# Kernel optimization log

Measured on AMD Instinct MI355X. Metric: run time of the kernel, lower is better.

The kernel has to match this reference:

```python
import jax, jax.numpy as jnp
import numpy as np
from jax import lax

H = 64
V = 32000
B = 32
T = 512


def setup_inputs() -> dict:
    key = jax.random.key(0)
    k1, k2, k3, k4 = jax.random.split(key, 4)
    # Parameters, constructed exactly as in SOHMM.__init__
    alpha_exp = jax.nn.softmax(jax.random.normal(k1, (H, H, H), dtype=jnp.float32), axis=2)
    beta = jax.nn.log_softmax(jax.random.normal(k2, (H, V), dtype=jnp.float32), axis=1)
    gamma = jax.nn.log_softmax(jax.random.normal(k3, (H, H), dtype=jnp.float32).reshape(-1)).reshape(H, H)
    input_ids = jax.random.randint(k4, (B, T), 0, V, dtype=jnp.int64)
    return {"alpha_exp": alpha_exp, "beta": beta, "gamma": gamma, "input_ids": input_ids}


def reference(alpha_exp, beta, gamma, input_ids):
    # input_ids: [B, T]
    h = alpha_exp.shape[0]
    b, t = input_ids.shape
    ids = input_ids.T  # [T, B]
    mask = (ids != -1)
    # emission log-probs per timestep: [T, H, B]; -1 padding tokens zeroed
    ip = jnp.transpose(beta[:, jnp.where(mask, ids, 0)], (1, 0, 2)) * mask[:, None, :].astype(beta.dtype)
    gamma_exp = jax.nn.softmax(gamma.reshape(-1)).reshape(gamma.shape)

    # t = T-1: y starts at zeros then adds emission
    y0 = jnp.zeros((h, h, b), dtype=beta.dtype) + ip[-1][None, :, :]

    def step(y, ip_t):
        y_max = y.max(axis=(0, 1), keepdims=True)            # [1,1,B]
        y_exp = jnp.exp(y - y_max)
        y = jnp.log(jnp.einsum('ijk,jkb->ijb', alpha_exp, y_exp)) + y_max
        y = y + ip_t[None, :, :]
        return y, y

    # loop t = T-2 .. 0 (reverse over remaining emissions)
    y_last, ys_rest = lax.scan(step, y0, ip[:-1][::-1])
    ys = jnp.concatenate([y0[None], ys_rest], axis=0)       # [T, H, H, B]

    y_max = y_last.max(axis=(0, 1))                          # [B]
    final = jnp.log(jnp.einsum('ij,ijb->b', gamma_exp, jnp.exp(y_last - y_max[None, None, :]))) + y_max
    return ys, final
```

## Files before the change

kernel.cpp:

```cpp
#include <hip/hip_runtime.h>
#include <cstdint>
#include <cstddef>

#define Hh 64
#define Vv 32000
#define Bb 32
#define Tt 512

typedef _Float16 half2_t __attribute__((ext_vector_type(2)));

#define IP_OFF    0ull
#define IP_SZ     ((size_t)Bb*Tt*Hh*4)
#define SL_OFF    (IP_OFF + IP_SZ)
#define SL_SZ     ((size_t)Bb*Tt*4)
#define DM_OFF    (SL_OFF + SL_SZ)
#define DM_SZ     ((size_t)Bb*Tt*4)
#define U511_OFF  (DM_OFF + DM_SZ)
#define U511_SZ   ((size_t)Bb*Hh*Hh*4)
#define STAGE_OFF (U511_OFF + U511_SZ)
#define STAGE_SZ  ((size_t)Tt*Bb*Hh*Hh*2)

__device__ __forceinline__ float wave_max64(float v){
  #pragma unroll
  for (int off=32; off; off>>=1) v = fmaxf(v, __shfl_xor(v, off, 64));
  return v;
}

__device__ __forceinline__ half2_t pk16(float x, float y){
  return __builtin_bit_cast(half2_t, __builtin_amdgcn_cvt_pkrtz(x, y));
}

__global__ __launch_bounds__(256) void sohmm_ipfill(
    const float* __restrict__ beta, const int* __restrict__ ids,
    float* __restrict__ ipbuf, float* __restrict__ dmax)
{
  const int bid = blockIdx.x;
  const int b = bid >> 7, tq = bid & 127;
  const int t = tq*4 + (threadIdx.x >> 6);
  const int j = threadIdx.x & 63;
  const int id = ids[b*Tt + t];
  float ip = beta[(size_t)j*Vv + id];
  ipbuf[((size_t)b*Tt + t)*Hh + j] = ip;
  float m = wave_max64(ip);
  if (j == 0) dmax[b*Tt + t] = m;
}

__global__ __launch_bounds__(512)
void sohmm_scan(
    const float* __restrict__ alpha, const float* __restrict__ ipbuf,
    const float* __restrict__ dmax,
    float* __restrict__ out, float* __restrict__ SL,
    float* __restrict__ u511, unsigned int* __restrict__ stage, int use_stage)
{
  const int b    = blockIdx.x;
  const int tid  = threadIdx.x;
  const int j    = tid >> 3;
  const int igrp = tid & 7;
  const int w    = tid >> 6;
  const int lane = tid & 63;
  const int i0   = igrp * 8;

  __shared__ char zb[2][64*128];
  __shared__ char aL[512*272];
  __shared__ float wred[2][8];

  half2_t areg[6][32];
  #pragma unroll
  for (int m=0; m<6; m++){
    const float4* ap = (const float4*)(alpha + (((size_t)(i0+m))*Hh + j)*Hh);
    #pragma unroll
    for (int q=0; q<16; q++){
      float4 v = ap[q];
      areg[m][2*q+0] = pk16(v.x, v.y);
      areg[m][2*q+1] = pk16(v.z, v.w);
    }
  }
  #pragma unroll
  for (int mm=0; mm<2; mm++){
    const float4* ap = (const float4*)(alpha + (((size_t)(i0+6+mm))*Hh + j)*Hh);
    #pragma unroll
    for (int q=0; q<8; q++){
      float4 v0 = ap[2*q], v1 = ap[2*q+1];
      uint4 u;
      u.x = __builtin_bit_cast(unsigned, __builtin_amdgcn_cvt_pkrtz(v0.x, v0.y));
      u.y = __builtin_bit_cast(unsigned, __builtin_amdgcn_cvt_pkrtz(v0.z, v0.w));
      u.z = __builtin_bit_cast(unsigned, __builtin_amdgcn_cvt_pkrtz(v1.x, v1.y));
      u.w = __builtin_bit_cast(unsigned, __builtin_amdgcn_cvt_pkrtz(v1.z, v1.w));
      *(uint4*)(aL + (size_t)tid*272 + mm*128 + q*16) = u;
    }
  }
  __syncthreads();

  const int kzj = ((j >> 3) ^ j) & 7;
  const int jc  = j >> 3;
  const int jo  = (j & 7) * 2;

  float logC = 0.f;

  for (int s=0; s<Tt; s++){
    const int cs = s & 1, ps = cs ^ 1;
    const int t  = (Tt-1) - s;

    float ipv = ipbuf[((size_t)b*Tt + t)*Hh + j];
    float dmv = dmax[b*Tt + t];

    float y[8];

    if (s){
      uint4 w0 = *(const uint4*)(&wred[ps][0]);
      uint4 w1 = *(const uint4*)(&wred[ps][4]);
      float Mprev = fmaxf(
        fmaxf(fmaxf(__uint_as_float(w0.x),__uint_as_float(w0.y)),
              fmaxf(__uint_as_float(w0.z),__uint_as_float(w0.w))),
        fmaxf(fmaxf(__uint_as_float(w1.x),__uint_as_float(w1.y)),
              fmaxf(__uint_as_float(w1.z),__uint_as_float(w1.w))));

      float acc[8];
      #pragma unroll
      for (int m=0;m<8;m++) acc[m] = 0.f;

      const char* zrow = zb[ps] + j*128;
      const char* arow = aL + (size_t)tid*272;
      #pragma unroll
      for (int h=0; h<2; h++){
        unsigned zz[16];
        #pragma unroll
        for (int c=0; c<4; c++){
          uint4 zq = *(const uint4*)(zrow + (((h*4+c) ^ kzj) << 4));
          zz[4*c+0]=zq.x; zz[4*c+1]=zq.y; zz[4*c+2]=zq.z; zz[4*c+3]=zq.w;
        }
        #pragma unroll
        for (int m=0; m<6; m++){
          #pragma unroll
          for (int p=0; p<16; p++)
            acc[m] = __builtin_amdgcn_fdot2(areg[m][16*h+p],
                       __builtin_bit_cast(half2_t, zz[p]), acc[m], false);
        }
        #pragma unroll
        for (int mm=0; mm<2; mm++){
          unsigned aa[16];
          #pragma unroll
          for (int c=0; c<4; c++){
            uint4 aq = *(const uint4*)(arow + mm*128 + h*64 + c*16);
            aa[4*c+0]=aq.x; aa[4*c+1]=aq.y; aa[4*c+2]=aq.z; aa[4*c+3]=aq.w;
          }
          #pragma unroll
          for (int p=0; p<16; p++)
            acc[6+mm] = __builtin_amdgcn_fdot2(__builtin_bit_cast(half2_t, aa[p]),
                           __builtin_bit_cast(half2_t, zz[p]), acc[6+mm], false);
        }
      }
      float scale = __expf(ipv - dmv) / Mprev;
      #pragma unroll
      for (int m=0;m<8;m++) y[m] = acc[m] * scale;
      logC += __logf(Mprev) + dmv;
    } else {
      float e = __expf(ipv - dmv);
      #pragma unroll
      for (int m=0;m<8;m++) y[m] = e;
      logC = dmv;
    }

    float vm = y[0];
    #pragma unroll
    for (int m=1;m<8;m++) vm = fmaxf(vm, y[m]);
    vm = wave_max64(vm);
    if (lane==0) wred[cs][w] = vm;

    if (tid==0) SL[(size_t)b*Tt + s] = logC;

    if (use_stage){
      unsigned pk4[4];
      #pragma unroll
      for (int q=0;q<4;q++)
        pk4[q] = (__float_as_uint(y[2*q]) >> 16) | (__float_as_uint(y[2*q+1]) & 0xFFFF0000u);
      uint4 o; o.x=pk4[0]; o.y=pk4[1]; o.z=pk4[2]; o.w=pk4[3];
      *(uint4*)(stage + ((size_t)s*Bb + b)*2048 + (size_t)j*32 + igrp*4) = o;
    } else {
      #pragma unroll
      for (int m=0;m<8;m++)
        out[(((size_t)s*Hh + (i0+m))*Hh + j)*Bb + b] = __logf(y[m]) + logC;
    }
    if (s == Tt-1){
      float4* ud = (float4*)(u511 + (size_t)b*4096 + (size_t)j*64 + i0);
      #pragma unroll
      for (int q=0;q<2;q++){
        float4 o; o.x=y[4*q]; o.y=y[4*q+1]; o.z=y[4*q+2]; o.w=y[4*q+3];
        ud[q] = o;
      }
    }

    {
      #pragma unroll
      for (int m=0;m<8;m++){
        int i = i0 + m;
        int ck = (jc ^ igrp ^ m) & 7;
        _Float16 hv = (_Float16)fmaxf(y[m], 1e-7f);
        *(short*)(zb[cs] + i*128 + (ck<<4) + jo) = __builtin_bit_cast(short, hv);
      }
    }

    __syncthreads();
  }
}

__global__ __launch_bounds__(256) void sohmm_emit(
    const unsigned short* __restrict__ stage, const float* __restrict__ SL,
    float* __restrict__ out)
{
  const int s  = blockIdx.x >> 3;
  const int jb = blockIdx.x & 7;
  const int tid = threadIdx.x;

  __shared__ unsigned short T[32*514];
  __shared__ float Sl[32];

  if (tid < 32) Sl[tid] = SL[(size_t)tid*Tt + s];

  #pragma unroll 4
  for (int bb=0; bb<32; bb++){
    ushort2 v = ((const ushort2*)(stage + ((size_t)s*Bb + bb)*4096 + (size_t)jb*512))[tid];
    *(ushort2*)(&T[bb*514 + tid*2]) = v;
  }
  __syncthreads();

  const int bch = tid & 31;
  const int pg  = tid >> 5;
  #pragma unroll 4
  for (int r=0; r<64; r++){
    int p  = r*8 + pg;
    int jr = p >> 6;
    int i  = p & 63;
    unsigned short h = T[bch*514 + jr*64 + i];
    float u = __uint_as_float(((unsigned)h) << 16);
    out[(((size_t)s*Hh + i)*Hh + (jb*8 + jr))*Bb + bch] = __logf(u) + Sl[bch];
  }
}

__global__ __launch_bounds__(256) void sohmm_final(
    const float* __restrict__ gamma, const float* __restrict__ u511,
    const float* __restrict__ SL, float* __restrict__ out)
{
  const int b = blockIdx.x, tid = threadIdx.x;
  const int w = tid>>6, lane = tid&63;
  __shared__ float red[4], red2[4];

  float gm = -3.4e38f;
  #pragma unroll
  for (int q=0;q<16;q++) gm = fmaxf(gm, gamma[q*256+tid]);
  gm = wave_max64(gm);
  if (lane==0) red[w] = gm;
  __syncthreads();
  gm = fmaxf(fmaxf(red[0],red[1]), fmaxf(red[2],red[3]));
  __syncthreads();

  float se=0.f, dot=0.f;
  #pragma unroll
  for (int q=0;q<16;q++){
    int idx = q*256+tid;
    int ii = idx>>6, jj = idx&63;
    float gq = __expf(gamma[idx]-gm);
    se  += gq;
    dot += gq * u511[(size_t)b*4096 + (size_t)jj*64 + ii];
  }
  #pragma unroll
  for (int off=32; off; off>>=1){
    se  += __shfl_xor(se,  off, 64);
    dot += __shfl_xor(dot, off, 64);
  }
  if (lane==0){ red[w]=se; red2[w]=dot; }
  __syncthreads();
  if (tid==0){
    float ses  = red[0]+red[1]+red[2]+red[3];
    float dots = red2[0]+red2[1]+red2[2]+red2[3];
    out[(size_t)Tt*Hh*Hh*Bb + b] = __logf(dots/ses) + SL[(size_t)b*Tt + (Tt-1)];
  }
}

extern "C" void kernel_launch(void* const* d_in, const int* in_sizes, int n_in,
                              void* d_out, int out_size, void* d_ws, size_t ws_size,
                              hipStream_t stream)
{
  (void)in_sizes; (void)n_in; (void)out_size;
  const float* alpha = (const float*)d_in[0];
  const float* beta  = (const float*)d_in[1];
  const float* gamma = (const float*)d_in[2];
  const int*   ids   = (const int*)d_in[3];
  float* out = (float*)d_out;
  char*  ws  = (char*)d_ws;

  float*          ipbuf = (float*)(ws + IP_OFF);
  float*          SLp   = (float*)(ws + SL_OFF);
  float*          dmaxp = (float*)(ws + DM_OFF);
  float*          u511p = (float*)(ws + U511_OFF);
  unsigned int*   stage = (unsigned int*)(ws + STAGE_OFF);

  const int use_stage = (ws_size >= STAGE_OFF + STAGE_SZ) ? 1 : 0;

  hipLaunchKernelGGL(sohmm_ipfill, dim3(Bb*128), dim3(256), 0, stream,
                     beta, ids, ipbuf, dmaxp);
  hipLaunchKernelGGL(sohmm_scan, dim3(Bb), dim3(512), 0, stream,
                     alpha, ipbuf, dmaxp, out, SLp, u511p, stage, use_stage);
  if (use_stage){
    hipLaunchKernelGGL(sohmm_emit, dim3(Tt*8), dim3(256), 0, stream,
                       (const unsigned short*)stage, SLp, out);
  }
  hipLaunchKernelGGL(sohmm_final, dim3(Bb), dim3(256), 0, stream,
                     gamma, u511p, SLp, out);
}
```

Baseline: 1.171 ms.

## Unroll scan loop by two with precomputed LDS pointers and DPP wave max

Restructures the sequential scan kernel's time loop. The first step is peeled, the rest is unrolled by two so the double-buffer index is a compile-time constant, and LDS read/write addresses and global pointers are precomputed and advanced incrementally. It also replaces the shuffle-based wave max with a DPP/row-broadcast reduction read from lane 63, swaps the division for a hardware reciprocal, and packs bf16 halves with v_perm. The aim is to shorten the per-step serial critical path in this latency-bound recurrence, at the cost of relying on exact DPP row_bcast semantics and a slightly less precise reciprocal.

```diff
diff --git a/kernel.cpp b/kernel.cpp
--- a/kernel.cpp
+++ b/kernel.cpp
@@ -30,6 +30,19 @@
   return __builtin_bit_cast(half2_t, __builtin_amdgcn_cvt_pkrtz(x, y));
 }
 
+#define DPP_MAXSTEP(v, CTRL) \
+  v = fmaxf(v, __int_as_float(__builtin_amdgcn_update_dpp(0, __float_as_int(v), CTRL, 0xF, 0xF, false)))
+
+__device__ __forceinline__ float wave_max_dpp63(float v){
+  DPP_MAXSTEP(v, 0xB1);
+  DPP_MAXSTEP(v, 0x4E);
+  DPP_MAXSTEP(v, 0x141);
+  DPP_MAXSTEP(v, 0x140);
+  DPP_MAXSTEP(v, 0x142);
+  DPP_MAXSTEP(v, 0x143);
+  return v;
+}
+
 __global__ __launch_bounds__(256) void sohmm_ipfill(
     const float* __restrict__ beta, const int* __restrict__ ids,
     float* __restrict__ ipbuf, float* __restrict__ dmax)
@@ -62,7 +75,7 @@
 
   __shared__ char zb[2][64*128];
   __shared__ char aL[512*272];
-  __shared__ float wred[2][8];
+  __shared__ __align__(16) float wred[2][8];
 
   half2_t areg[6][32];
   #pragma unroll
@@ -95,112 +108,137 @@
   const int jc  = j >> 3;
   const int jo  = (j & 7) * 2;
 
-  float logC = 0.f;
-
-  for (int s=0; s<Tt; s++){
-    const int cs = s & 1, ps = cs ^ 1;
-    const int t  = (Tt-1) - s;
-
-    float ipv = ipbuf[((size_t)b*Tt + t)*Hh + j];
-    float dmv = dmax[b*Tt + t];
-
-    float y[8];
-
-    if (s){
-      uint4 w0 = *(const uint4*)(&wred[ps][0]);
-      uint4 w1 = *(const uint4*)(&wred[ps][4]);
-      float Mprev = fmaxf(
-        fmaxf(fmaxf(__uint_as_float(w0.x),__uint_as_float(w0.y)),
-              fmaxf(__uint_as_float(w0.z),__uint_as_float(w0.w))),
-        fmaxf(fmaxf(__uint_as_float(w1.x),__uint_as_float(w1.y)),
-              fmaxf(__uint_as_float(w1.z),__uint_as_float(w1.w))));
-
-      float acc[8];
-      #pragma unroll
-      for (int m=0;m<8;m++) acc[m] = 0.f;
-
-      const char* zrow = zb[ps] + j*128;
-      const char* arow = aL + (size_t)tid*272;
-      #pragma unroll
-      for (int h=0; h<2; h++){
-        unsigned zz[16];
-        #pragma unroll
-        for (int c=0; c<4; c++){
-          uint4 zq = *(const uint4*)(zrow + (((h*4+c) ^ kzj) << 4));
-          zz[4*c+0]=zq.x; zz[4*c+1]=zq.y; zz[4*c+2]=zq.z; zz[4*c+3]=zq.w;
-        }
-        #pragma unroll
-        for (int m=0; m<6; m++){
-          #pragma unroll
-          for (int p=0; p<16; p++)
-            acc[m] = __builtin_amdgcn_fdot2(areg[m][16*h+p],
-                       __builtin_bit_cast(half2_t, zz[p]), acc[m], false);
-        }
-        #pragma unroll
-        for (int mm=0; mm<2; mm++){
-          unsigned aa[16];
-          #pragma unroll
-          for (int c=0; c<4; c++){
-            uint4 aq = *(const uint4*)(arow + mm*128 + h*64 + c*16);
-            aa[4*c+0]=aq.x; aa[4*c+1]=aq.y; aa[4*c+2]=aq.z; aa[4*c+3]=aq.w;
-          }
-          #pragma unroll
-          for (int p=0; p<16; p++)
-            acc[6+mm] = __builtin_amdgcn_fdot2(__builtin_bit_cast(half2_t, aa[p]),
-                           __builtin_bit_cast(half2_t, zz[p]), acc[6+mm], false);
-        }
-      }
-      float scale = __expf(ipv - dmv) / Mprev;
-      #pragma unroll
-      for (int m=0;m<8;m++) y[m] = acc[m] * scale;
-      logC += __logf(Mprev) + dmv;
-    } else {
-      float e = __expf(ipv - dmv);
-      #pragma unroll
-      for (int m=0;m<8;m++) y[m] = e;
-      logC = dmv;
-    }
-
-    float vm = y[0];
-    #pragma unroll
-    for (int m=1;m<8;m++) vm = fmaxf(vm, y[m]);
-    vm = wave_max64(vm);
-    if (lane==0) wred[cs][w] = vm;
-
-    if (tid==0) SL[(size_t)b*Tt + s] = logC;
-
+  const char* zr0[8];
+  char*       zw0[8];
+  #pragma unroll
+  for (int c=0;c<8;c++) zr0[c] = zb[0] + j*128 + ((c ^ kzj) << 4);
+  #pragma unroll
+  for (int m=0;m<8;m++) zw0[m] = zb[0] + (i0+m)*128 + (((jc ^ igrp ^ m) & 7) << 4) + jo;
+  const char* arow = aL + (size_t)tid*272;
+
+  const float* ipp = ipbuf + (size_t)b*Tt*Hh + (size_t)(Tt-1)*Hh + j;
+  const float* dmp = dmax + b*Tt + (Tt-1);
+  float*       slp = SL + (size_t)b*Tt;
+  unsigned*    stg = stage + (size_t)b*2048 + (size_t)j*32 + igrp*4;
+  float*       outp = out + (((size_t)i0)*Hh + j)*Bb + b;
+
+  float y[8];
+  float logC;
+
+  {
+    float ipv = *ipp; ipp -= Hh;
+    float dmv = *dmp; dmp -= 1;
+    float e = __expf(ipv - dmv);
+    #pragma unroll
+    for (int m=0;m<8;m++) y[m] = e;
+    logC = dmv;
+    float vm = wave_max_dpp63(e);
+    if (lane==63) wred[0][w] = vm;
+    if (tid==0) slp[0] = logC;
     if (use_stage){
       unsigned pk4[4];
       #pragma unroll
       for (int q=0;q<4;q++)
-        pk4[q] = (__float_as_uint(y[2*q]) >> 16) | (__float_as_uint(y[2*q+1]) & 0xFFFF0000u);
+        pk4[q] = __builtin_amdgcn_perm(__float_as_uint(y[2*q+1]), __float_as_uint(y[2*q]), 0x07060302);
       uint4 o; o.x=pk4[0]; o.y=pk4[1]; o.z=pk4[2]; o.w=pk4[3];
-      *(uint4*)(stage + ((size_t)s*Bb + b)*2048 + (size_t)j*32 + igrp*4) = o;
+      *(uint4*)stg = o;
     } else {
       #pragma unroll
-      for (int m=0;m<8;m++)
-        out[(((size_t)s*Hh + (i0+m))*Hh + j)*Bb + b] = __logf(y[m]) + logC;
-    }
-    if (s == Tt-1){
-      float4* ud = (float4*)(u511 + (size_t)b*4096 + (size_t)j*64 + i0);
-      #pragma unroll
-      for (int q=0;q<2;q++){
-        float4 o; o.x=y[4*q]; o.y=y[4*q+1]; o.z=y[4*q+2]; o.w=y[4*q+3];
-        ud[q] = o;
-      }
-    }
-
-    {
-      #pragma unroll
-      for (int m=0;m<8;m++){
-        int i = i0 + m;
-        int ck = (jc ^ igrp ^ m) & 7;
-        _Float16 hv = (_Float16)fmaxf(y[m], 1e-7f);
-        *(short*)(zb[cs] + i*128 + (ck<<4) + jo) = __builtin_bit_cast(short, hv);
-      }
-    }
-
+      for (int m=0;m<8;m++) outp[(size_t)m*Hh*Bb] = __logf(y[m]) + logC;
+    }
+    stg += Bb*2048; outp += (size_t)Hh*Hh*Bb;
+    #pragma unroll
+    for (int m=0;m<8;m++){
+      _Float16 hv = (_Float16)fmaxf(y[m], 1e-7f);
+      *(short*)(zw0[m]) = __builtin_bit_cast(short, hv);
+    }
     __syncthreads();
+  }
+
+#define STEP(CS) { \
+    float ipv = *ipp; ipp -= Hh; \
+    float dmv = *dmp; dmp -= 1; \
+    slp += 1; \
+    uint4 q0 = *(const uint4*)(&wred[CS^1][0]); \
+    uint4 q1 = *(const uint4*)(&wred[CS^1][4]); \
+    float Mp = fmaxf( \
+      fmaxf(fmaxf(__uint_as_float(q0.x),__uint_as_float(q0.y)), \
+            fmaxf(__uint_as_float(q0.z),__uint_as_float(q0.w))), \
+      fmaxf(fmaxf(__uint_as_float(q1.x),__uint_as_float(q1.y)), \
+            fmaxf(__uint_as_float(q1.z),__uint_as_float(q1.w)))); \
+    float acc[8]; \
+    _Pragma("unroll") for (int m=0;m<8;m++) acc[m] = 0.f; \
+    _Pragma("unroll") \
+    for (int h=0; h<2; h++){ \
+      unsigned zz[16]; \
+      _Pragma("unroll") \
+      for (int c=0; c<4; c++){ \
+        uint4 zq = *(const uint4*)(zr0[h*4+c] + (CS^1)*8192); \
+        zz[4*c+0]=zq.x; zz[4*c+1]=zq.y; zz[4*c+2]=zq.z; zz[4*c+3]=zq.w; \
+      } \
+      _Pragma("unroll") \
+      for (int m=0; m<6; m++){ \
+        _Pragma("unroll") \
+        for (int p=0; p<16; p++) \
+          acc[m] = __builtin_amdgcn_fdot2(areg[m][16*h+p], \
+                     __builtin_bit_cast(half2_t, zz[p]), acc[m], false); \
+      } \
+      _Pragma("unroll") \
+      for (int mm=0; mm<2; mm++){ \
+        unsigned aa[16]; \
+        _Pragma("unroll") \
+        for (int c=0; c<4; c++){ \
+          uint4 aq = *(const uint4*)(arow + mm*128 + h*64 + c*16); \
+          aa[4*c+0]=aq.x; aa[4*c+1]=aq.y; aa[4*c+2]=aq.z; aa[4*c+3]=aq.w; \
+        } \
+        _Pragma("unroll") \
+        for (int p=0; p<16; p++) \
+          acc[6+mm] = __builtin_amdgcn_fdot2(__builtin_bit_cast(half2_t, aa[p]), \
+                         __builtin_bit_cast(half2_t, zz[p]), acc[6+mm], false); \
+      } \
+    } \
+    float scale = __expf(ipv - dmv) * __builtin_amdgcn_rcpf(Mp); \
+    _Pragma("unroll") for (int m=0;m<8;m++) y[m] = acc[m]*scale; \
+    logC += __logf(Mp) + dmv; \
+    float vm = fmaxf(fmaxf(fmaxf(y[0],y[1]),fmaxf(y[2],y[3])), \
+                     fmaxf(fmaxf(y[4],y[5]),fmaxf(y[6],y[7]))); \
+    vm = wave_max_dpp63(vm); \
+    if (lane==63) wred[CS][w] = vm; \
+    if (tid==0) *slp = logC; \
+    if (use_stage){ \
+      unsigned pk4[4]; \
+      _Pragma("unroll") \
+      for (int q=0;q<4;q++) \
+        pk4[q] = __builtin_amdgcn_perm(__float_as_uint(y[2*q+1]), __float_as_uint(y[2*q]), 0x07060302); \
+      uint4 o; o.x=pk4[0]; o.y=pk4[1]; o.z=pk4[2]; o.w=pk4[3]; \
+      *(uint4*)stg = o; \
+    } else { \
+      _Pragma("unroll") \
+      for (int m=0;m<8;m++) outp[(size_t)m*Hh*Bb] = __logf(y[m]) + logC; \
+    } \
+    stg += Bb*2048; outp += (size_t)Hh*Hh*Bb; \
+    _Pragma("unroll") \
+    for (int m=0;m<8;m++){ \
+      _Float16 hv = (_Float16)fmaxf(y[m], 1e-7f); \
+      *(short*)(zw0[m] + (CS)*8192) = __builtin_bit_cast(short, hv); \
+    } \
+    __syncthreads(); \
+  }
+
+  for (int sp=0; sp<255; sp++){
+    STEP(1)
+    STEP(0)
+  }
+  STEP(1)
+#undef STEP
+
+  {
+    float4* ud = (float4*)(u511 + (size_t)b*4096 + (size_t)j*64 + i0);
+    #pragma unroll
+    for (int q=0;q<2;q++){
+      float4 o; o.x=y[4*q]; o.y=y[4*q+1]; o.z=y[4*q+2]; o.w=y[4*q+3];
+      ud[q] = o;
+    }
   }
 }
 
```

Result: faster. 1.074 ms (median of 2 runs) (-8.3%).
